# Kernel tuning notes

Measured on AMD Instinct MI355X. Metric: run time of the kernel, lower is better.

Reference implementation:

```python
import jax, jax.numpy as jnp
import numpy as np

N_NODES = 100000
N_EDGES = 1600000
IN_FEATS = 128
H_FEATS = 64
NEG_SLOPE = 0.2


def gat_layer(x, W, a_l, a_r, b, src, dst):
    # x: [N, Fin], W: [Fin, Fout], a_l/a_r/b: [Fout]
    h = x @ W                                   # [N, Fout]
    el = h @ a_l                                # [N]
    er = h @ a_r                                # [N]
    e = el[src] + er[dst]                       # [E]
    e = jnp.where(e > 0, e, NEG_SLOPE * e)      # leaky_relu
    # segment softmax over incoming edges of each dst node
    m = jax.ops.segment_max(e, dst, num_segments=N_NODES)   # [N], -inf for deg-0
    ex = jnp.exp(e - m[dst])                                 # [E]
    s = jax.ops.segment_sum(ex, dst, num_segments=N_NODES)   # [N]
    alpha = ex / s[dst]                                      # [E]
    out = jax.ops.segment_sum(alpha[:, None] * h[src], dst, num_segments=N_NODES)
    return jax.nn.relu(out + b)


def setup_inputs() -> dict:
    key = jax.random.key(0)
    ks = jax.random.split(key, 16)
    in_feat = jax.random.normal(ks[0], (N_NODES, IN_FEATS), dtype=jnp.float32)
    src = jax.random.randint(ks[1], (N_EDGES,), 0, N_NODES, dtype=jnp.int32)
    dst = jax.random.randint(ks[2], (N_EDGES,), 0, N_NODES, dtype=jnp.int32)
    def w(k, fin, fout):
        return jax.random.normal(k, (fin, fout), dtype=jnp.float32) * (1.0 / np.sqrt(fin))
    def v(k, f):
        return jax.random.normal(k, (f,), dtype=jnp.float32) * 0.1
    return {
        "in_feat": in_feat, "src": src, "dst": dst,
        "W1": w(ks[3], IN_FEATS, H_FEATS), "al1": v(ks[4], H_FEATS), "ar1": v(ks[5], H_FEATS), "b1": jnp.zeros((H_FEATS,), jnp.float32),
        "W2": w(ks[6], H_FEATS, H_FEATS), "al2": v(ks[7], H_FEATS), "ar2": v(ks[8], H_FEATS), "b2": jnp.zeros((H_FEATS,), jnp.float32),
        "W3": w(ks[9], H_FEATS, H_FEATS), "al3": v(ks[10], H_FEATS), "ar3": v(ks[11], H_FEATS), "b3": jnp.zeros((H_FEATS,), jnp.float32),
    }


def reference(in_feat, src, dst, W1, al1, ar1, b1, W2, al2, ar2, b2, W3, al3, ar3, b3):
    h = gat_layer(in_feat, W1, al1, ar1, b1, src, dst)
    h = gat_layer(h, W2, al2, ar2, b2, src, dst)
    h = gat_layer(h, W3, al3, ar3, b3, src, dst)
    return h
```

## Files before the change

### kernel.cpp

```cpp
#include <hip/hip_runtime.h>
#include <hip/hip_fp16.h>
#include <math.h>

#define HF 64
#define LEAKY 0.2f
#define NBLK 256
#define NPB 512
#define MAXNB 256

typedef _Float16 f16x2 __attribute__((ext_vector_type(2)));

__device__ __forceinline__ float dot2f(f16x2 a, f16x2 b, float c) {
#if __has_builtin(__builtin_amdgcn_fdot2)
    return __builtin_amdgcn_fdot2(a, b, c, false);
#else
    return fmaf((float)a[0], (float)b[0], fmaf((float)a[1], (float)b[1], c));
#endif
}


__global__ __launch_bounds__(256)
void part_count(const int* __restrict__ dst, int* __restrict__ Cmat, int E, int nb) {
    __shared__ int lc[MAXNB];
    int tid = threadIdx.x;
    for (int t = tid; t < nb; t += 256) lc[t] = 0;
    __syncthreads();
    int chunk = (E + NBLK - 1) / NBLK;
    int b0 = blockIdx.x * chunk, b1 = min(b0 + chunk, E);
    for (int i = b0 + tid; i < b1; i += 256)
        atomicAdd(&lc[dst[i] >> 9], 1);
    __syncthreads();
    for (int t = tid; t < nb; t += 256) Cmat[t * NBLK + blockIdx.x] = lc[t];
}

__global__ __launch_bounds__(256)
void scan_offsets(const int* __restrict__ Cmat, int* __restrict__ Omat,
                  int* __restrict__ bbase, int E, int nb) {
    __shared__ int tot[256];
    int t = threadIdx.x;
    int s = 0;
    if (t < nb)
        for (int blk = 0; blk < NBLK; ++blk) s += Cmat[t * NBLK + blk];
    tot[t] = s;
    __syncthreads();
    for (int off = 1; off < 256; off <<= 1) {
        int u = (t >= off) ? tot[t - off] : 0;
        __syncthreads();
        tot[t] += u;
        __syncthreads();
    }
    int excl = tot[t] - s;
    if (t < nb) {
        bbase[t] = excl;
        int run = excl;
        for (int blk = 0; blk < NBLK; ++blk) {
            Omat[t * NBLK + blk] = run;
            run += Cmat[t * NBLK + blk];
        }
    }
    if (t == 0) bbase[nb] = E;
}

__global__ __launch_bounds__(256)
void part_scatter(const int* __restrict__ src, const int* __restrict__ dst,
                  const int* __restrict__ Omat, int2* __restrict__ part, int E, int nb) {
    __shared__ int ocur[MAXNB];
    int tid = threadIdx.x;
    for (int t = tid; t < nb; t += 256) ocur[t] = Omat[t * NBLK + blockIdx.x];
    __syncthreads();
    int chunk = (E + NBLK - 1) / NBLK;
    int b0 = blockIdx.x * chunk, b1 = min(b0 + chunk, E);
    for (int i = b0 + tid; i < b1; i += 256) {
        int s = src[i], d = dst[i];
        int pos = atomicAdd(&ocur[d >> 9], 1);
        part[pos] = make_int2(s, d);
    }
}

__global__ __launch_bounds__(NPB)
void bucket_csr(const int2* __restrict__ part, const int* __restrict__ bbase,
                int* __restrict__ row_ptr, int* __restrict__ ssrc, int N, int E, int nb) {
    int b = blockIdx.x, tid = threadIdx.x;
    int bstart = bbase[b], bend = bbase[b + 1];
    int nb0 = b << 9;
    __shared__ int cnt[NPB];
    cnt[tid] = 0;
    __syncthreads();
    for (int i = bstart + tid; i < bend; i += NPB)
        atomicAdd(&cnt[part[i].y & (NPB - 1)], 1);
    __syncthreads();
    int v = cnt[tid];
    for (int off = 1; off < NPB; off <<= 1) {
        int u = (tid >= off) ? cnt[tid - off] : 0;
        __syncthreads();
        cnt[tid] += u;
        __syncthreads();
    }
    int excl = cnt[tid] - v;
    int node = nb0 + tid;
    if (node < N) row_ptr[node] = bstart + excl;
    __syncthreads();
    cnt[tid] = bstart + excl;
    __syncthreads();
    for (int i = bstart + tid; i < bend; i += NPB) {
        int2 e = part[i];
        int slot = atomicAdd(&cnt[e.y & (NPB - 1)], 1);
        ssrc[slot] = e.x;
    }
    if (b == nb - 1 && tid == 0) row_ptr[N] = E;
}


template <int K>
__global__ __launch_bounds__(256)
void gemm_kernel(const float* __restrict__ X, const float* __restrict__ W,
                 const float* __restrict__ al, const float* __restrict__ ar,
                 __half* __restrict__ H2, float* __restrict__ el, float* __restrict__ er,
                 int n) {
    constexpr int K2 = K / 2;
    __shared__ f16x2 Wh[K2 * 64];
    __shared__ f16x2 Xh[64 * K2];
    int tid = threadIdx.x;
    int r0blk = blockIdx.x * 64;

    for (int idx = tid; idx < K2 * 64; idx += 256) {
        int k2 = idx >> 6, c = idx & 63;
        f16x2 h;
        h[0] = (_Float16)W[(2 * k2) * 64 + c];
        h[1] = (_Float16)W[(2 * k2 + 1) * 64 + c];
        Wh[idx] = h;
    }
    const float* Xg = X + (size_t)r0blk * K;
    for (int idx = tid; idx < 64 * (K / 4); idx += 256) {
        int row = idx / (K / 4), k4 = idx % (K / 4);
        float4 v = make_float4(0.f, 0.f, 0.f, 0.f);
        if (r0blk + row < n) v = *(const float4*)(Xg + (size_t)row * K + k4 * 4);
        f16x2 h0, h1;
        h0[0] = (_Float16)v.x; h0[1] = (_Float16)v.y;
        h1[0] = (_Float16)v.z; h1[1] = (_Float16)v.w;
        int sw = (row & 15) << 1;
        Xh[row * K2 + ((2 * k4) ^ sw)] = h0;
        Xh[row * K2 + ((2 * k4 + 1) ^ sw)] = h1;
    }
    __syncthreads();

    int tc = tid & 15, tr = tid >> 4;
    int r0 = r0blk + tr * 4;
    float acc[4][4] = {};

#pragma unroll 4
    for (int k2 = 0; k2 < K2; k2 += 2) {
        f16x2 xa[4], xb[4];
#pragma unroll
        for (int r = 0; r < 4; ++r) {
            int row = tr * 4 + r;
            int sw = (row & 15) << 1;
            const f16x2* p = &Xh[row * K2 + (k2 ^ sw)];
            xa[r] = p[0];
            xb[r] = p[1];
        }
        const f16x2* w0 = &Wh[k2 * 64 + tc * 4];
        const f16x2* w1 = &Wh[(k2 + 1) * 64 + tc * 4];
#pragma unroll
        for (int i = 0; i < 4; ++i) {
            f16x2 wv0 = w0[i], wv1 = w1[i];
#pragma unroll
            for (int r = 0; r < 4; ++r) {
                acc[r][i] = dot2f(xa[r], wv0, acc[r][i]);
                acc[r][i] = dot2f(xb[r], wv1, acc[r][i]);
            }
        }
    }

    float alv[4], arv[4];
#pragma unroll
    for (int i = 0; i < 4; ++i) { alv[i] = al[tc * 4 + i]; arv[i] = ar[tc * 4 + i]; }

#pragma unroll
    for (int r = 0; r < 4; ++r) {
        if (r0 + r >= n) continue;
        __half2 h01 = __floats2half2_rn(acc[r][0], acc[r][1]);
        __half2 h23 = __floats2half2_rn(acc[r][2], acc[r][3]);
        uint2 u = make_uint2(*(unsigned*)&h01, *(unsigned*)&h23);
        ((uint2*)(H2 + (size_t)(r0 + r) * HF))[tc] = u;
        float pl = acc[r][0] * alv[0] + acc[r][1] * alv[1] + acc[r][2] * alv[2] + acc[r][3] * alv[3];
        float pr = acc[r][0] * arv[0] + acc[r][1] * arv[1] + acc[r][2] * arv[2] + acc[r][3] * arv[3];
#pragma unroll
        for (int off = 1; off < 16; off <<= 1) {
            pl += __shfl_xor(pl, off);
            pr += __shfl_xor(pr, off);
        }
        if (tc == 0) { el[r0 + r] = pl; er[r0 + r] = pr; }
    }
}

__device__ __forceinline__
void node_fullwave(int node, const int* __restrict__ row_ptr, const int* __restrict__ ssrc,
                   const float* __restrict__ el, const float* __restrict__ er,
                   const uint2* __restrict__ H2v, const __half* __restrict__ H2,
                   float4 bv, const float* __restrict__ b, float* __restrict__ Y,
                   int lane, int g, int fl) {
    int s0 = row_ptr[node], s1 = row_ptr[node + 1];
    int d = s1 - s0;
    float ern = er[node];

    if (d <= 64) {
        int sidx = 0;
        float e = -INFINITY;
        if (lane < d) {
            sidx = ssrc[s0 + lane];
            e = el[sidx] + ern;
            e = e > 0.f ? e : LEAKY * e;
        }
        float m = e;
#pragma unroll
        for (int off = 32; off; off >>= 1) m = fmaxf(m, __shfl_xor(m, off));
        float p = (lane < d) ? __expf(e - m) : 0.f;
        float psum = p;
#pragma unroll
        for (int off = 32; off; off >>= 1) psum += __shfl_xor(psum, off);

        float4 acc = make_float4(0.f, 0.f, 0.f, 0.f);
        int nchunk = (d + 31) >> 5;
        for (int c = 0; c < nchunk; ++c) {
            int jb = c * 32 + g;
            int ss[8];
            float pp[8];
#pragma unroll
            for (int u = 0; u < 8; ++u) {
                ss[u] = __shfl(sidx, jb + 4 * u);
                pp[u] = __shfl(p, jb + 4 * u);
            }
            uint2 vv[8];
#pragma unroll
            for (int u = 0; u < 8; ++u) vv[u] = H2v[(size_t)ss[u] * 16 + fl];
#pragma unroll
            for (int u = 0; u < 8; ++u) {
                __half2 a = *(__half2*)&vv[u].x;
                __half2 b2 = *(__half2*)&vv[u].y;
                float2 fa = __half22float2(a);
                float2 fb = __half22float2(b2);
                acc.x = fmaf(pp[u], fa.x, acc.x);
                acc.y = fmaf(pp[u], fa.y, acc.y);
                acc.z = fmaf(pp[u], fb.x, acc.z);
                acc.w = fmaf(pp[u], fb.y, acc.w);
            }
        }
#pragma unroll
        for (int off = 16; off <= 32; off <<= 1) {
            acc.x += __shfl_xor(acc.x, off);
            acc.y += __shfl_xor(acc.y, off);
            acc.z += __shfl_xor(acc.z, off);
            acc.w += __shfl_xor(acc.w, off);
        }
        float inv = d ? 1.f / psum : 0.f;
        float4 o;
        o.x = fmaf(acc.x, inv, bv.x);
        o.y = fmaf(acc.y, inv, bv.y);
        o.z = fmaf(acc.z, inv, bv.z);
        o.w = fmaf(acc.w, inv, bv.w);
        o.x = o.x > 0.f ? o.x : 0.f;
        o.y = o.y > 0.f ? o.y : 0.f;
        o.z = o.z > 0.f ? o.z : 0.f;
        o.w = o.w > 0.f ? o.w : 0.f;
        if (g == 0) ((float4*)Y)[(size_t)node * 16 + fl] = o;
    } else {
        float m = -INFINITY;
        for (int j = s0 + lane; j < s1; j += 64) {
            float e = el[ssrc[j]] + ern;
            e = e > 0.f ? e : LEAKY * e;
            m = fmaxf(m, e);
        }
#pragma unroll
        for (int off = 32; off; off >>= 1) m = fmaxf(m, __shfl_xor(m, off));
        float acc = 0.f, psum = 0.f;
        for (int j = s0; j < s1; ++j) {
            int s = ssrc[j];
            float e = el[s] + ern;
            e = e > 0.f ? e : LEAKY * e;
            float p = __expf(e - m);
            psum += p;
            acc = fmaf(p, __half2float(H2[(size_t)s * HF + lane]), acc);
        }
        float o = acc / psum + b[lane];
        Y[(size_t)node * HF + lane] = o > 0.f ? o : 0.f;
    }
}

__global__ __launch_bounds__(256)
void edge_kernel(const int* __restrict__ row_ptr, const int* __restrict__ ssrc,
                 const float* __restrict__ el, const float* __restrict__ er,
                 const __half* __restrict__ H2, const float* __restrict__ b,
                 float* __restrict__ Y, int n) {
    int wave = threadIdx.x >> 6, lane = threadIdx.x & 63;
    int half = lane >> 5, hl = lane & 31;
    int g = lane >> 4, fl = lane & 15;
    const uint2* H2v = (const uint2*)H2;
    float4 bv = ((const float4*)b)[fl];
    int npairs = (n + 1) >> 1;

    for (int pr = blockIdx.x * 4 + wave; pr < npairs; pr += gridDim.x * 4) {
        int nodeA = pr * 2;
        int myNode = nodeA + half;
        bool ok = myNode < n;
        int s0 = 0, d = 0;
        if (ok) {
            s0 = row_ptr[myNode];
            d = row_ptr[myNode + 1] - s0;
        }
        int dA = __shfl(d, 0), dB = __shfl(d, 32);

        if (dA <= 32 && dB <= 32) {
            float ern = ok ? er[myNode] : 0.f;
            int sidx = 0;
            float e = -INFINITY;
            if (hl < d) {
                sidx = ssrc[s0 + hl];
                e = el[sidx] + ern;
                e = e > 0.f ? e : LEAKY * e;
            }
            float m = e;
#pragma unroll
            for (int off = 16; off; off >>= 1) m = fmaxf(m, __shfl_xor(m, off));
            float p = (hl < d) ? __expf(e - m) : 0.f;
            float psum = p;
#pragma unroll
            for (int off = 16; off; off >>= 1) psum += __shfl_xor(psum, off);

            float4 acc = make_float4(0.f, 0.f, 0.f, 0.f);
            int dg = (g >> 1) ? dB : dA;
            int hbase = (g >> 1) << 5;
            int gpar = g & 1;
            int nch = (dg + 15) >> 4;
            for (int c = 0; c < nch; ++c) {
                int ss[8];
                float pp[8];
#pragma unroll
                for (int u = 0; u < 8; ++u) {
                    int sl = hbase + c * 16 + 2 * u + gpar;
                    ss[u] = __shfl(sidx, sl);
                    pp[u] = __shfl(p, sl);
                }
                uint2 vv[8];
#pragma unroll
                for (int u = 0; u < 8; ++u) vv[u] = H2v[(size_t)ss[u] * 16 + fl];
#pragma unroll
                for (int u = 0; u < 8; ++u) {
                    __half2 a = *(__half2*)&vv[u].x;
                    __half2 b2 = *(__half2*)&vv[u].y;
                    float2 fa = __half22float2(a);
                    float2 fb = __half22float2(b2);
                    acc.x = fmaf(pp[u], fa.x, acc.x);
                    acc.y = fmaf(pp[u], fa.y, acc.y);
                    acc.z = fmaf(pp[u], fb.x, acc.z);
                    acc.w = fmaf(pp[u], fb.y, acc.w);
                }
            }
            acc.x += __shfl_xor(acc.x, 16);
            acc.y += __shfl_xor(acc.y, 16);
            acc.z += __shfl_xor(acc.z, 16);
            acc.w += __shfl_xor(acc.w, 16);
            float inv = d ? 1.f / psum : 0.f;
            float4 o;
            o.x = fmaf(acc.x, inv, bv.x);
            o.y = fmaf(acc.y, inv, bv.y);
            o.z = fmaf(acc.z, inv, bv.z);
            o.w = fmaf(acc.w, inv, bv.w);
            o.x = o.x > 0.f ? o.x : 0.f;
            o.y = o.y > 0.f ? o.y : 0.f;
            o.z = o.z > 0.f ? o.z : 0.f;
            o.w = o.w > 0.f ? o.w : 0.f;
            if (!(g & 1) && ok) ((float4*)Y)[(size_t)myNode * 16 + fl] = o;
        } else {
            node_fullwave(nodeA, row_ptr, ssrc, el, er, H2v, H2, bv, b, Y, lane, g, fl);
            if (nodeA + 1 < n)
                node_fullwave(nodeA + 1, row_ptr, ssrc, el, er, H2v, H2, bv, b, Y, lane, g, fl);
        }
    }
}


extern "C" void kernel_launch(void* const* d_in, const int* in_sizes, int n_in,
                              void* d_out, int out_size, void* d_ws, size_t ws_size,
                              hipStream_t stream) {
    const int N = in_sizes[0] / 128;
    const int E = in_sizes[1];
    const int nb = (N + NPB - 1) >> 9;

    const float* in_feat = (const float*)d_in[0];
    const int* src = (const int*)d_in[1];
    const int* dst = (const int*)d_in[2];
    const float* W1 = (const float*)d_in[3];
    const float* al1 = (const float*)d_in[4];
    const float* ar1 = (const float*)d_in[5];
    const float* b1 = (const float*)d_in[6];
    const float* W2 = (const float*)d_in[7];
    const float* al2 = (const float*)d_in[8];
    const float* ar2 = (const float*)d_in[9];
    const float* b2 = (const float*)d_in[10];
    const float* W3 = (const float*)d_in[11];
    const float* al3 = (const float*)d_in[12];
    const float* ar3 = (const float*)d_in[13];
    const float* b3 = (const float*)d_in[14];

    char* ws = (char*)d_ws;
    size_t off = 0;
    auto alloc = [&](size_t bytes) {
        void* p = ws + off;
        off += (bytes + 255) & ~(size_t)255;
        return p;
    };
    int* row_ptr = (int*)alloc(((size_t)N + 1) * 4);
    int* ssrc = (int*)alloc((size_t)E * 4);
    int2* part = (int2*)alloc((size_t)E * 8);
    int* Cmat = (int*)alloc((size_t)MAXNB * NBLK * 4);
    int* Omat = (int*)alloc((size_t)MAXNB * NBLK * 4);
    int* bbase = (int*)alloc(((size_t)MAXNB + 1) * 4);
    float* el = (float*)alloc((size_t)N * 4);
    float* er = (float*)alloc((size_t)N * 4);
    __half* H2buf = (__half*)alloc((size_t)N * HF * 2);
    float* Ybuf = (float*)alloc((size_t)N * HF * 4);

    part_count<<<NBLK, 256, 0, stream>>>(dst, Cmat, E, nb);
    scan_offsets<<<1, 256, 0, stream>>>(Cmat, Omat, bbase, E, nb);
    part_scatter<<<NBLK, 256, 0, stream>>>(src, dst, Omat, part, E, nb);
    bucket_csr<<<nb, NPB, 0, stream>>>(part, bbase, row_ptr, ssrc, N, E, nb);

    int gt = (N + 63) / 64;
    int ge = 2048;

    gemm_kernel<128><<<gt, 256, 0, stream>>>(in_feat, W1, al1, ar1, H2buf, el, er, N);
    edge_kernel<<<ge, 256, 0, stream>>>(row_ptr, ssrc, el, er, H2buf, b1, Ybuf, N);
    gemm_kernel<64><<<gt, 256, 0, stream>>>(Ybuf, W2, al2, ar2, H2buf, el, er, N);
    edge_kernel<<<ge, 256, 0, stream>>>(row_ptr, ssrc, el, er, H2buf, b2, Ybuf, N);
    gemm_kernel<64><<<gt, 256, 0, stream>>>(Ybuf, W3, al3, ar3, H2buf, el, er, N);
    edge_kernel<<<ge, 256, 0, stream>>>(row_ptr, ssrc, el, er, H2buf, b3, (float*)d_out, N);
}
```

Before: 265.0 us.

## Store intermediate activations in fp16 and make GEMM persistent with double-buffered tiles

Intermediate layer outputs are now written as fp16 by the edge kernel and read directly as fp16 by the next layer's GEMM. This halves the bytes moved between layers. The GEMM becomes persistent: each block handles about three 64-row tiles, loads weights once, and prefetches the next tile's X into registers while computing the current one, using a double-buffered shared tile. This adds an extra fp16 rounding of activations, which the GEMM already did internally, and reduces the grid size, which may lower occupancy.

```diff
diff --git a/kernel.cpp b/kernel.cpp
--- a/kernel.cpp
+++ b/kernel.cpp
@@ -111,17 +111,22 @@
 }
 
 
-template <int K>
+template <int K, bool XF16>
 __global__ __launch_bounds__(256)
-void gemm_kernel(const float* __restrict__ X, const float* __restrict__ W,
+void gemm_kernel(const void* __restrict__ Xv, const float* __restrict__ W,
                  const float* __restrict__ al, const float* __restrict__ ar,
                  __half* __restrict__ H2, float* __restrict__ el, float* __restrict__ er,
-                 int n) {
+                 int n, int ntiles) {
     constexpr int K2 = K / 2;
+    constexpr int F4 = K / 4;
+    constexpr int NL = 64 * F4 / 256;
     __shared__ f16x2 Wh[K2 * 64];
-    __shared__ f16x2 Xh[64 * K2];
+    __shared__ f16x2 Xh[2][64 * K2];
     int tid = threadIdx.x;
-    int r0blk = blockIdx.x * 64;
+
+    int tpb = (ntiles + gridDim.x - 1) / gridDim.x;
+    int t0 = blockIdx.x * tpb, t1 = min(t0 + tpb, ntiles);
+    if (t0 >= t1) return;
 
     for (int idx = tid; idx < K2 * 64; idx += 256) {
         int k2 = idx >> 6, c = idx & 63;
@@ -130,75 +135,114 @@
         h[1] = (_Float16)W[(2 * k2 + 1) * 64 + c];
         Wh[idx] = h;
     }
-    const float* Xg = X + (size_t)r0blk * K;
-    for (int idx = tid; idx < 64 * (K / 4); idx += 256) {
-        int row = idx / (K / 4), k4 = idx % (K / 4);
-        float4 v = make_float4(0.f, 0.f, 0.f, 0.f);
-        if (r0blk + row < n) v = *(const float4*)(Xg + (size_t)row * K + k4 * 4);
-        f16x2 h0, h1;
-        h0[0] = (_Float16)v.x; h0[1] = (_Float16)v.y;
-        h1[0] = (_Float16)v.z; h1[1] = (_Float16)v.w;
-        int sw = (row & 15) << 1;
-        Xh[row * K2 + ((2 * k4) ^ sw)] = h0;
-        Xh[row * K2 + ((2 * k4 + 1) ^ sw)] = h1;
-    }
-    __syncthreads();
+
+    float4 xregf[XF16 ? 1 : NL];
+    uint2 xregh[XF16 ? NL : 1];
+
+    auto load_regs = [&](int t) {
+        int rb = t * 64;
+#pragma unroll
+        for (int j = 0; j < NL; ++j) {
+            int idx = tid + j * 256;
+            int row = idx / F4;
+            bool ok = rb + row < n;
+            if constexpr (XF16) {
+                uint2 z = make_uint2(0u, 0u);
+                xregh[j] = ok ? ((const uint2*)Xv)[(size_t)rb * (K / 4) + idx] : z;
+            } else {
+                float4 z = make_float4(0.f, 0.f, 0.f, 0.f);
+                xregf[j] = ok ? ((const float4*)Xv)[(size_t)rb * (K / 4) + idx] : z;
+            }
+        }
+    };
+    auto store_X = [&](int buf) {
+#pragma unroll
+        for (int j = 0; j < NL; ++j) {
+            int idx = tid + j * 256;
+            int row = idx / F4, k4 = idx % F4;
+            int sw = (row & 15) << 1;
+            f16x2 h0, h1;
+            if constexpr (XF16) {
+                h0 = *(f16x2*)&xregh[j].x;
+                h1 = *(f16x2*)&xregh[j].y;
+            } else {
+                h0[0] = (_Float16)xregf[j].x; h0[1] = (_Float16)xregf[j].y;
+                h1[0] = (_Float16)xregf[j].z; h1[1] = (_Float16)xregf[j].w;
+            }
+            Xh[buf][row * K2 + ((2 * k4) ^ sw)] = h0;
+            Xh[buf][row * K2 + ((2 * k4 + 1) ^ sw)] = h1;
+        }
+    };
 
     int tc = tid & 15, tr = tid >> 4;
-    int r0 = r0blk + tr * 4;
-    float acc[4][4] = {};
-
+    float alv[4], arv[4];
+#pragma unroll
+    for (int i = 0; i < 4; ++i) { alv[i] = al[tc * 4 + i]; arv[i] = ar[tc * 4 + i]; }
+
+    load_regs(t0);
+    store_X(0);
+    __syncthreads();
+    int cur = 0;
+
+    for (int t = t0; t < t1; ++t) {
+        bool pf = (t + 1 < t1);
+        if (pf) load_regs(t + 1);
+
+        float acc[4][4] = {};
 #pragma unroll 4
-    for (int k2 = 0; k2 < K2; k2 += 2) {
-        f16x2 xa[4], xb[4];
+        for (int k2 = 0; k2 < K2; k2 += 2) {
+            f16x2 xa[4], xb[4];
+#pragma unroll
+            for (int r = 0; r < 4; ++r) {
+                int row = tr * 4 + r;
+                int sw = (row & 15) << 1;
+                const f16x2* p = &Xh[cur][row * K2 + (k2 ^ sw)];
+                xa[r] = p[0];
+                xb[r] = p[1];
+            }
+            const f16x2* w0 = &Wh[k2 * 64 + tc * 4];
+            const f16x2* w1 = &Wh[(k2 + 1) * 64 + tc * 4];
+#pragma unroll
+            for (int i = 0; i < 4; ++i) {
+                f16x2 wv0 = w0[i], wv1 = w1[i];
+#pragma unroll
+                for (int r = 0; r < 4; ++r) {
+                    acc[r][i] = dot2f(xa[r], wv0, acc[r][i]);
+                    acc[r][i] = dot2f(xb[r], wv1, acc[r][i]);
+                }
+            }
+        }
+
+        int r0 = t * 64 + tr * 4;
 #pragma unroll
         for (int r = 0; r < 4; ++r) {
-            int row = tr * 4 + r;
-            int sw = (row & 15) << 1;
-            const f16x2* p = &Xh[row * K2 + (k2 ^ sw)];
-            xa[r] = p[0];
-            xb[r] = p[1];
-        }
-        const f16x2* w0 = &Wh[k2 * 64 + tc * 4];
-        const f16x2* w1 = &Wh[(k2 + 1) * 64 + tc * 4];
-#pragma unroll
-        for (int i = 0; i < 4; ++i) {
-            f16x2 wv0 = w0[i], wv1 = w1[i];
-#pragma unroll
-            for (int r = 0; r < 4; ++r) {
-                acc[r][i] = dot2f(xa[r], wv0, acc[r][i]);
-                acc[r][i] = dot2f(xb[r], wv1, acc[r][i]);
-            }
-        }
-    }
-
-    float alv[4], arv[4];
-#pragma unroll
-    for (int i = 0; i < 4; ++i) { alv[i] = al[tc * 4 + i]; arv[i] = ar[tc * 4 + i]; }
-
-#pragma unroll
-    for (int r = 0; r < 4; ++r) {
-        if (r0 + r >= n) continue;
-        __half2 h01 = __floats2half2_rn(acc[r][0], acc[r][1]);
-        __half2 h23 = __floats2half2_rn(acc[r][2], acc[r][3]);
-        uint2 u = make_uint2(*(unsigned*)&h01, *(unsigned*)&h23);
-        ((uint2*)(H2 + (size_t)(r0 + r) * HF))[tc] = u;
-        float pl = acc[r][0] * alv[0] + acc[r][1] * alv[1] + acc[r][2] * alv[2] + acc[r][3] * alv[3];
-        float pr = acc[r][0] * arv[0] + acc[r][1] * arv[1] + acc[r][2] * arv[2] + acc[r][3] * arv[3];
-#pragma unroll
-        for (int off = 1; off < 16; off <<= 1) {
-            pl += __shfl_xor(pl, off);
-            pr += __shfl_xor(pr, off);
-        }
-        if (tc == 0) { el[r0 + r] = pl; er[r0 + r] = pr; }
-    }
-}
-
+            if (r0 + r >= n) continue;
+            __half2 h01 = __floats2half2_rn(acc[r][0], acc[r][1]);
+            __half2 h23 = __floats2half2_rn(acc[r][2], acc[r][3]);
+            uint2 u = make_uint2(*(unsigned*)&h01, *(unsigned*)&h23);
+            ((uint2*)(H2 + (size_t)(r0 + r) * HF))[tc] = u;
+            float pl = acc[r][0] * alv[0] + acc[r][1] * alv[1] + acc[r][2] * alv[2] + acc[r][3] * alv[3];
+            float pr = acc[r][0] * arv[0] + acc[r][1] * arv[1] + acc[r][2] * arv[2] + acc[r][3] * arv[3];
+#pragma unroll
+            for (int off = 1; off < 16; off <<= 1) {
+                pl += __shfl_xor(pl, off);
+                pr += __shfl_xor(pr, off);
+            }
+            if (tc == 0) { el[r0 + r] = pl; er[r0 + r] = pr; }
+        }
+
+        if (pf) store_X(cur ^ 1);
+        __syncthreads();
+        if (pf) cur ^= 1;
+    }
+}
+
+template <bool YF16>
 __device__ __forceinline__
 void node_fullwave(int node, const int* __restrict__ row_ptr, const int* __restrict__ ssrc,
                    const float* __restrict__ el, const float* __restrict__ er,
                    const uint2* __restrict__ H2v, const __half* __restrict__ H2,
-                   float4 bv, const float* __restrict__ b, float* __restrict__ Y,
+                   float4 bv, const float* __restrict__ b, void* __restrict__ Y,
                    int lane, int g, int fl) {
     int s0 = row_ptr[node], s1 = row_ptr[node + 1];
     int d = s1 - s0;
@@ -263,7 +307,15 @@
         o.y = o.y > 0.f ? o.y : 0.f;
         o.z = o.z > 0.f ? o.z : 0.f;
         o.w = o.w > 0.f ? o.w : 0.f;
-        if (g == 0) ((float4*)Y)[(size_t)node * 16 + fl] = o;
+        if (g == 0) {
+            if constexpr (YF16) {
+                __half2 a = __floats2half2_rn(o.x, o.y);
+                __half2 c = __floats2half2_rn(o.z, o.w);
+                ((uint2*)Y)[(size_t)node * 16 + fl] = make_uint2(*(unsigned*)&a, *(unsigned*)&c);
+            } else {
+                ((float4*)Y)[(size_t)node * 16 + fl] = o;
+            }
+        }
     } else {
         float m = -INFINITY;
         for (int j = s0 + lane; j < s1; j += 64) {
@@ -283,15 +335,20 @@
             acc = fmaf(p, __half2float(H2[(size_t)s * HF + lane]), acc);
         }
         float o = acc / psum + b[lane];
-        Y[(size_t)node * HF + lane] = o > 0.f ? o : 0.f;
-    }
-}
-
+        o = o > 0.f ? o : 0.f;
+        if constexpr (YF16)
+            ((__half*)Y)[(size_t)node * HF + lane] = __float2half(o);
+        else
+            ((float*)Y)[(size_t)node * HF + lane] = o;
+    }
+}
+
+template <bool YF16>
 __global__ __launch_bounds__(256)
 void edge_kernel(const int* __restrict__ row_ptr, const int* __restrict__ ssrc,
                  const float* __restrict__ el, const float* __restrict__ er,
                  const __half* __restrict__ H2, const float* __restrict__ b,
-                 float* __restrict__ Y, int n) {
+                 void* __restrict__ Y, int n) {
     int wave = threadIdx.x >> 6, lane = threadIdx.x & 63;
     int half = lane >> 5, hl = lane & 31;
     int g = lane >> 4, fl = lane & 15;
@@ -370,11 +427,19 @@
             o.y = o.y > 0.f ? o.y : 0.f;
             o.z = o.z > 0.f ? o.z : 0.f;
             o.w = o.w > 0.f ? o.w : 0.f;
-            if (!(g & 1) && ok) ((float4*)Y)[(size_t)myNode * 16 + fl] = o;
+            if (!(g & 1) && ok) {
+                if constexpr (YF16) {
+                    __half2 a = __floats2half2_rn(o.x, o.y);
+                    __half2 c2 = __floats2half2_rn(o.z, o.w);
+                    ((uint2*)Y)[(size_t)myNode * 16 + fl] = make_uint2(*(unsigned*)&a, *(unsigned*)&c2);
+                } else {
+                    ((float4*)Y)[(size_t)myNode * 16 + fl] = o;
+                }
+            }
         } else {
-            node_fullwave(nodeA, row_ptr, ssrc, el, er, H2v, H2, bv, b, Y, lane, g, fl);
+            node_fullwave<YF16>(nodeA, row_ptr, ssrc, el, er, H2v, H2, bv, b, Y, lane, g, fl);
             if (nodeA + 1 < n)
-                node_fullwave(nodeA + 1, row_ptr, ssrc, el, er, H2v, H2, bv, b, Y, lane, g, fl);
+                node_fullwave<YF16>(nodeA + 1, row_ptr, ssrc, el, er, H2v, H2, bv, b, Y, lane, g, fl);
         }
     }
 }
@@ -419,20 +484,21 @@
     float* el = (float*)alloc((size_t)N * 4);
     float* er = (float*)alloc((size_t)N * 4);
     __half* H2buf = (__half*)alloc((size_t)N * HF * 2);
-    float* Ybuf = (float*)alloc((size_t)N * HF * 4);
+    __half* Y2buf = (__half*)alloc((size_t)N * HF * 2);
 
     part_count<<<NBLK, 256, 0, stream>>>(dst, Cmat, E, nb);
     scan_offsets<<<1, 256, 0, stream>>>(Cmat, Omat, bbase, E, nb);
     part_scatter<<<NBLK, 256, 0, stream>>>(src, dst, Omat, part, E, nb);
     bucket_csr<<<nb, NPB, 0, stream>>>(part, bbase, row_ptr, ssrc, N, E, nb);
 
-    int gt = (N + 63) / 64;
+    int ntiles = (N + 63) / 64;
+    int gg = (ntiles + 2) / 3;
     int ge = 2048;
 
-    gemm_kernel<128><<<gt, 256, 0, stream>>>(in_feat, W1, al1, ar1, H2buf, el, er, N);
-    edge_kernel<<<ge, 256, 0, stream>>>(row_ptr, ssrc, el, er, H2buf, b1, Ybuf, N);
-    gemm_kernel<64><<<gt, 256, 0, stream>>>(Ybuf, W2, al2, ar2, H2buf, el, er, N);
-    edge_kernel<<<ge, 256, 0, stream>>>(row_ptr, ssrc, el, er, H2buf, b2, Ybuf, N);
-    gemm_kernel<64><<<gt, 256, 0, stream>>>(Ybuf, W3, al3, ar3, H2buf, el, er, N);
-    edge_kernel<<<ge, 256, 0, stream>>>(row_ptr, ssrc, el, er, H2buf, b3, (float*)d_out, N);
-}
+    gemm_kernel<128, false><<<gg, 256, 0, stream>>>(in_feat, W1, al1, ar1, H2buf, el, er, N, ntiles);
+    edge_kernel<true><<<ge, 256, 0, stream>>>(row_ptr, ssrc, el, er, H2buf, b1, Y2buf, N);
+    gemm_kernel<64, true><<<gg, 256, 0, stream>>>(Y2buf, W2, al2, ar2, H2buf, el, er, N, ntiles);
+    edge_kernel<true><<<ge, 256, 0, stream>>>(row_ptr, ssrc, el, er, H2buf, b2, Y2buf, N);
+    gemm_kernel<64, true><<<gg, 256, 0, stream>>>(Y2buf, W3, al3, ar3, H2buf, el, er, N, ntiles);
+    edge_kernel<false><<<ge, 256, 0, stream>>>(row_ptr, ssrc, el, er, H2buf, b3, d_out, N);
+}
```

New measurement: 281.1 us. +6.1%, slower.
